# Kernel optimization log

Hardware: AMD Instinct MI355X
Metric: run time of the kernel (lower is better)

Reference implementation:

```python
import jax, jax.numpy as jnp
import numpy as np

B, C, H, W = 4, 128, 64, 64
NUM_HEADS = 4
HEAD_DIM = C // NUM_HEADS


def setup_inputs() -> dict:
    key = jax.random.key(0)
    ks = jax.random.split(key, 9)
    s = 0.02
    return {
        "x": jax.random.normal(ks[0], (B, C, H, W), dtype=jnp.float32),
        "wq": jax.random.normal(ks[1], (C, C), dtype=jnp.float32) * s,
        "bq": jax.random.normal(ks[2], (C,), dtype=jnp.float32) * s,
        "wk": jax.random.normal(ks[3], (C, C), dtype=jnp.float32) * s,
        "bk": jax.random.normal(ks[4], (C,), dtype=jnp.float32) * s,
        "wv": jax.random.normal(ks[5], (C, C), dtype=jnp.float32) * s,
        "bv": jax.random.normal(ks[6], (C,), dtype=jnp.float32) * s,
        "wo": jax.random.normal(ks[7], (C, C), dtype=jnp.float32) * s,
        "bo": jax.random.normal(ks[8], (C,), dtype=jnp.float32) * s,
    }


def _proj(w, b, xf):
    # 1x1 conv == channel-mixing linear: xf is (B, C, N)
    return jnp.einsum("oc,bcn->bon", w, xf) + b[None, :, None]


def reference(x, wq, bq, wk, bk, wv, bv, wo, bo):
    b, c, h, w = x.shape
    n = h * w
    nh, hd = NUM_HEADS, HEAD_DIM
    xf = x.reshape(b, c, n)
    q = _proj(wq, bq, xf).reshape(b, nh, hd, n)
    k = _proj(wk, bk, xf).reshape(b, nh, hd, n)
    v = _proj(wv, bv, xf).reshape(b, nh, hd, n)
    # scores: (b, heads, n, n)
    scores = jnp.einsum("bhdn,bhdm->bhnm", q, k) / jnp.sqrt(jnp.float32(hd)).astype(x.dtype)
    prob = jax.nn.softmax(scores, axis=-1)
    # attn_out: (b, heads, head_dim, n)
    attn = jnp.einsum("bhnm,bhdm->bhdn", prob, v).reshape(b, c, n)
    out = _proj(wo, bo, attn).reshape(b, c, h, w)
    return x + out
```

## Files before the change

### kernel.cpp

```cpp
#include <hip/hip_runtime.h>
#include <hip/hip_bf16.h>

#define BB 4
#define CC 128
#define NN 4096
#define NHEAD 4
#define HDIM 32
#define KSPLIT 2

typedef short bf16x8_t __attribute__((ext_vector_type(8)));
typedef float f32x4_t __attribute__((ext_vector_type(4)));
typedef int i32x4_t __attribute__((ext_vector_type(4)));

#define MFMA16(a, b, c) __builtin_amdgcn_mfma_f32_16x16x32_bf16(a, b, c, 0, 0, 0)
#define EXP2(x) __builtin_amdgcn_exp2f(x)

#define QSCALE (0.17677669529663687f * 1.4426950408889634f)

static __device__ inline unsigned short f2bf(float f) {
  unsigned u = __builtin_bit_cast(unsigned, f);
  u += 0x7fffu + ((u >> 16) & 1u);
  return (unsigned short)(u >> 16);
}
static __device__ inline unsigned pk2(float lo, float hi) {
  return (unsigned)f2bf(lo) | ((unsigned)f2bf(hi) << 16);
}
static __device__ inline unsigned pack_trunc(float lo, float hi) {
  return __builtin_amdgcn_perm(__builtin_bit_cast(unsigned, hi),
                               __builtin_bit_cast(unsigned, lo), 0x07060302u);
}

static __device__ inline void gload_lds16(const unsigned short* gsrc, void* ldst) {
  __builtin_amdgcn_global_load_lds(
      (const __attribute__((address_space(1))) unsigned int*)gsrc,
      (__attribute__((address_space(3))) unsigned int*)ldst, 16, 0, 0);
}

__global__ __launch_bounds__(256) void wconv_kernel(
    const float* __restrict__ wq, const float* __restrict__ wk,
    const float* __restrict__ wv, const float* __restrict__ wo,
    unsigned short* __restrict__ wb) {
  int f = (blockIdx.x * 256 + threadIdx.x) * 8;
  int m = f >> 14, off = f & 16383;
  const float* src = (m == 0) ? wq : (m == 1) ? wk : (m == 2) ? wv : wo;
  float sc = (m == 0) ? QSCALE : 1.0f;
  float4 a = *(const float4*)(src + off);
  float4 b = *(const float4*)(src + off + 4);
  ushort4 u0, u1;
  u0.x = f2bf(a.x * sc); u0.y = f2bf(a.y * sc); u0.z = f2bf(a.z * sc); u0.w = f2bf(a.w * sc);
  u1.x = f2bf(b.x * sc); u1.y = f2bf(b.y * sc); u1.z = f2bf(b.z * sc); u1.w = f2bf(b.w * sc);
  *(ushort4*)(wb + f) = u0;
  *(ushort4*)(wb + f + 4) = u1;
}

__global__ __launch_bounds__(256) void qkv_mfma_kernel(
    const float* __restrict__ x,
    const unsigned short* __restrict__ wqb, const unsigned short* __restrict__ wkb,
    const unsigned short* __restrict__ wvb,
    const float* __restrict__ bq, const float* __restrict__ bk,
    const float* __restrict__ bv,
    unsigned short* __restrict__ qt, unsigned short* __restrict__ kt,
    unsigned short* __restrict__ vg) {
  __shared__ __attribute__((aligned(16))) unsigned short xsb[64][136];
  __shared__ unsigned short vt[128][66];
  const int b = blockIdx.y, nt = blockIdx.x, proj = blockIdx.z;
  const int tid = threadIdx.x;

#pragma unroll
  for (int i = 0; i < 8; i++) {
    int f = tid + 256 * i;
    int c = f >> 4, n4 = (f & 15) * 4;
    float4 v4 = *(const float4*)(x + ((size_t)b * CC + c) * NN + nt * 64 + n4);
    xsb[n4 + 0][c] = f2bf(v4.x);
    xsb[n4 + 1][c] = f2bf(v4.y);
    xsb[n4 + 2][c] = f2bf(v4.z);
    xsb[n4 + 3][c] = f2bf(v4.w);
  }
  __syncthreads();

  const int lane = tid & 63, w = tid >> 6;
  const int l16 = lane & 15, g = lane >> 4;
  const int nl = w * 16;
  const int ngl = nt * 64 + nl;

  bf16x8_t xf[4];
#pragma unroll
  for (int ks = 0; ks < 4; ks++)
    xf[ks] = *(const bf16x8_t*)&xsb[nl + l16][ks * 32 + g * 8];

  const unsigned short* wm = (proj == 0) ? wqb : (proj == 1) ? wkb : wvb;
  const float* bias = (proj == 0) ? bq : (proj == 1) ? bk : bv;
  const float bsc = (proj == 0) ? QSCALE : 1.0f;
  unsigned short* qkdst = proj ? kt : qt;

#pragma unroll
  for (int ot = 0; ot < 8; ot++) {
    f32x4_t acc;
#pragma unroll
    for (int r = 0; r < 4; r++) acc[r] = bias[ot * 16 + g * 4 + r] * bsc;
#pragma unroll
    for (int ks = 0; ks < 4; ks++) {
      bf16x8_t wf = *(const bf16x8_t*)(wm + (size_t)(ot * 16 + l16) * CC + ks * 32 + g * 8);
      acc = MFMA16(wf, xf[ks], acc);
    }
    if (proj < 2) {
      unsigned p0 = pk2(acc[0], acc[1]);
      unsigned p1 = pk2(acc[2], acc[3]);
      unsigned q0 = (unsigned)__shfl_xor((int)p0, 16);
      unsigned q1 = (unsigned)__shfl_xor((int)p1, 16);
      if ((g & 1) == 0) {
        int hh = ot >> 1, dblk = (ot & 1) * 2 + (g >> 1);
        unsigned short* dst =
            qkdst + (((size_t)(b * NHEAD + hh) * 4 + dblk) * NN + ngl + l16) * 8;
        uint4 val = make_uint4(p0, p1, q0, q1);
        *(uint4*)dst = val;
      }
    } else {
#pragma unroll
      for (int r = 0; r < 4; r++) vt[ot * 16 + g * 4 + r][nl + l16] = f2bf(acc[r]);
    }
  }

  if (proj == 2) {
    __syncthreads();
#pragma unroll
    for (int c = 0; c < 4; c++) {
      int cid = c * 256 + tid;
      int hh = cid >> 8, inner = cid & 255;
      int g2 = inner & 3, l16v = (inner >> 2) & 15, fh = inner >> 6;
      int fv = fh >> 1, half = fh & 1;
      int o = hh * 32 + half * 16 + l16v;
      int n0 = fv * 32 + g2 * 4;
      unsigned d0 = *(const unsigned*)&vt[o][n0];
      unsigned d1 = *(const unsigned*)&vt[o][n0 + 2];
      unsigned d2 = *(const unsigned*)&vt[o][n0 + 16];
      unsigned d3 = *(const unsigned*)&vt[o][n0 + 18];
      uint4 val = make_uint4(d0, d1, d2, d3);
      *(uint4*)(vg + (((size_t)(b * NHEAD + hh) * 64 + nt) * 256 + inner) * 8) = val;
    }
  }
}

__global__ __launch_bounds__(256, 4) void attn_mfma5_kernel(
    const unsigned short* __restrict__ qt, const unsigned short* __restrict__ kt,
    const unsigned short* __restrict__ vg,
    float* __restrict__ opart, float* __restrict__ lpart) {
  __shared__ __attribute__((aligned(16))) unsigned short smem[2][4096];

  const int chunk = blockIdx.x & (KSPLIT - 1), nt = blockIdx.x / KSPLIT;
  const int h = blockIdx.y, b = blockIdx.z;
  const int bh = b * NHEAD + h;
  const int tid = threadIdx.x, lane = tid & 63, wid = tid >> 6;
  const int l16 = lane & 15, g = lane >> 4;
  const int nbase = nt * 128 + wid * 32;

  const unsigned short* qb = qt + (size_t)bh * NN * HDIM;
  const unsigned short* kb = kt + (size_t)bh * NN * HDIM;
  const unsigned short* vgb = vg + (size_t)bh * 64 * 2048;

  const bf16x8_t qf0 = *(const bf16x8_t*)(qb + ((size_t)g * NN + nbase + l16) * 8);
  const bf16x8_t qf1 = *(const bf16x8_t*)(qb + ((size_t)g * NN + nbase + 16 + l16) * 8);

  f32x4_t o00 = {0, 0, 0, 0}, o01 = {0, 0, 0, 0};
  f32x4_t o10 = {0, 0, 0, 0}, o11 = {0, 0, 0, 0};
  f32x4_t la = {0, 0, 0, 0}, lb = {0, 0, 0, 0};
  const f32x4_t zf = {0, 0, 0, 0};
  const i32x4_t onesi = {0x3F803F80, 0x3F803F80, 0x3F803F80, 0x3F803F80};
  const bf16x8_t ones = __builtin_bit_cast(bf16x8_t, onesi);

  const int NITER = 64 / KSPLIT;
  const int mt0 = chunk * NITER;

  const unsigned short* ksrc = kb + ((size_t)g * NN + mt0 * 64 + wid * 16 + l16) * 8;
  const unsigned short* vsrc = vgb + (size_t)mt0 * 2048 + (size_t)((wid * 16 + l16) * 4 + g) * 8;

  auto stage = [&](int p, int i) {
    gload_lds16(ksrc + (size_t)i * 512, &smem[p][wid * 512]);
    gload_lds16(vsrc + (size_t)i * 2048, &smem[p][2048 + wid * 512]);
  };

  auto body = [&](int p) {
    const unsigned short* sk = &smem[p][0];
    bf16x8_t k0 = *(const bf16x8_t*)(sk + 0 * 512 + lane * 8);
    bf16x8_t k1 = *(const bf16x8_t*)(sk + 1 * 512 + lane * 8);
    bf16x8_t k2 = *(const bf16x8_t*)(sk + 2 * 512 + lane * 8);
    bf16x8_t k3 = *(const bf16x8_t*)(sk + 3 * 512 + lane * 8);
    bf16x8_t vf0 = *(const bf16x8_t*)(sk + 2048 + 0 * 512 + lane * 8);
    bf16x8_t vf2 = *(const bf16x8_t*)(sk + 2048 + 1 * 512 + lane * 8);
    bf16x8_t vf1 = *(const bf16x8_t*)(sk + 2048 + 2 * 512 + lane * 8);
    bf16x8_t vf3 = *(const bf16x8_t*)(sk + 2048 + 3 * 512 + lane * 8);

    f32x4_t sA0 = MFMA16(k0, qf0, zf), sA1 = MFMA16(k1, qf0, zf);
    f32x4_t sA2 = MFMA16(k2, qf0, zf), sA3 = MFMA16(k3, qf0, zf);
    f32x4_t sB0 = MFMA16(k0, qf1, zf), sB1 = MFMA16(k1, qf1, zf);
    f32x4_t sB2 = MFMA16(k2, qf1, zf), sB3 = MFMA16(k3, qf1, zf);

#pragma unroll
    for (int r = 0; r < 4; r++) {
      sA0[r] = EXP2(sA0[r]); sA1[r] = EXP2(sA1[r]);
      sA2[r] = EXP2(sA2[r]); sA3[r] = EXP2(sA3[r]);
      sB0[r] = EXP2(sB0[r]); sB1[r] = EXP2(sB1[r]);
      sB2[r] = EXP2(sB2[r]); sB3[r] = EXP2(sB3[r]);
    }

    i32x4_t pA0i = {(int)pack_trunc(sA0[0], sA0[1]), (int)pack_trunc(sA0[2], sA0[3]),
                    (int)pack_trunc(sA1[0], sA1[1]), (int)pack_trunc(sA1[2], sA1[3])};
    i32x4_t pA1i = {(int)pack_trunc(sA2[0], sA2[1]), (int)pack_trunc(sA2[2], sA2[3]),
                    (int)pack_trunc(sA3[0], sA3[1]), (int)pack_trunc(sA3[2], sA3[3])};
    i32x4_t pB0i = {(int)pack_trunc(sB0[0], sB0[1]), (int)pack_trunc(sB0[2], sB0[3]),
                    (int)pack_trunc(sB1[0], sB1[1]), (int)pack_trunc(sB1[2], sB1[3])};
    i32x4_t pB1i = {(int)pack_trunc(sB2[0], sB2[1]), (int)pack_trunc(sB2[2], sB2[3]),
                    (int)pack_trunc(sB3[0], sB3[1]), (int)pack_trunc(sB3[2], sB3[3])};
    bf16x8_t pA0 = __builtin_bit_cast(bf16x8_t, pA0i);
    bf16x8_t pA1 = __builtin_bit_cast(bf16x8_t, pA1i);
    bf16x8_t pB0 = __builtin_bit_cast(bf16x8_t, pB0i);
    bf16x8_t pB1 = __builtin_bit_cast(bf16x8_t, pB1i);

    o00 = MFMA16(vf0, pA0, o00); o00 = MFMA16(vf1, pA1, o00);
    o01 = MFMA16(vf2, pA0, o01); o01 = MFMA16(vf3, pA1, o01);
    o10 = MFMA16(vf0, pB0, o10); o10 = MFMA16(vf1, pB1, o10);
    o11 = MFMA16(vf2, pB0, o11); o11 = MFMA16(vf3, pB1, o11);

    la = MFMA16(ones, pA0, la); la = MFMA16(ones, pA1, la);
    lb = MFMA16(ones, pB0, lb); lb = MFMA16(ones, pB1, lb);
  };

  stage(0, 0);
  __syncthreads();
  for (int mi = 0; mi < NITER; mi += 2) {
    stage(1, mi + 1);
    body(0);
    __syncthreads();
    if (mi + 2 < NITER) stage(0, mi + 2);
    body(1);
    __syncthreads();
  }

  float* obase = opart + ((size_t)(chunk * BB * NHEAD + bh)) * HDIM * NN;
#pragma unroll
  for (int r = 0; r < 4; r++) {
    obase[(size_t)(g * 4 + r) * NN + nbase + l16] = o00[r];
    obase[(size_t)(16 + g * 4 + r) * NN + nbase + l16] = o01[r];
    obase[(size_t)(g * 4 + r) * NN + nbase + 16 + l16] = o10[r];
    obase[(size_t)(16 + g * 4 + r) * NN + nbase + 16 + l16] = o11[r];
  }
  if (g == 0) {
    float* lb_ = lpart + (size_t)(chunk * BB * NHEAD + bh) * NN;
    lb_[nbase + l16] = la[0];
    lb_[nbase + 16 + l16] = lb[0];
  }
}

__global__ __launch_bounds__(256) void combine_kernel(
    const float* __restrict__ opart, const float* __restrict__ lpart,
    unsigned short* __restrict__ attnT) {
  const int n = blockIdx.x * 256 + threadIdx.x;
  const int bh = blockIdx.y, dg = blockIdx.z;
  const int b = bh >> 2, h = bh & 3;

  float l = 0.f;
#pragma unroll
  for (int c = 0; c < KSPLIT; c++) l += lpart[(size_t)(c * BB * NHEAD + bh) * NN + n];
  float inv = 1.f / l;

  unsigned dw[4];
#pragma unroll
  for (int p = 0; p < 4; p++) {
    float s0 = 0.f, s1 = 0.f;
#pragma unroll
    for (int c = 0; c < KSPLIT; c++) {
      const float* ob = opart + ((size_t)(c * BB * NHEAD + bh) * HDIM + dg * 8) * NN;
      s0 += ob[(size_t)(2 * p) * NN + n];
      s1 += ob[(size_t)(2 * p + 1) * NN + n];
    }
    dw[p] = (unsigned)f2bf(s0 * inv) | ((unsigned)f2bf(s1 * inv) << 16);
  }
  unsigned short* dst = attnT + ((size_t)b * NN + n) * CC + h * HDIM + dg * 8;
  *(uint4*)dst = *(uint4*)&dw[0];
}

__global__ __launch_bounds__(256) void out_mfma_kernel(
    const unsigned short* __restrict__ attnT, const unsigned short* __restrict__ wob,
    const float* __restrict__ bo, const float* __restrict__ x,
    float* __restrict__ out) {
  const int b = blockIdx.y, nt = blockIdx.x, quarter = blockIdx.z;
  const int tid = threadIdx.x, lane = tid & 63, w = tid >> 6;
  const int l16 = lane & 15, g = lane >> 4;
  const int n0 = nt * 64 + w * 16;

  bf16x8_t bf[4];
#pragma unroll
  for (int ks = 0; ks < 4; ks++)
    bf[ks] = *(const bf16x8_t*)(attnT + ((size_t)b * NN + n0 + l16) * CC + ks * 32 + g * 8);

#pragma unroll
  for (int mi = 0; mi < 2; mi++) {
    int mt = quarter * 2 + mi;
    f32x4_t acc;
#pragma unroll
    for (int r = 0; r < 4; r++) acc[r] = bo[mt * 16 + g * 4 + r];
#pragma unroll
    for (int ks = 0; ks < 4; ks++) {
      bf16x8_t af = *(const bf16x8_t*)(wob + (size_t)(mt * 16 + l16) * CC + ks * 32 + g * 8);
      acc = MFMA16(af, bf[ks], acc);
    }
#pragma unroll
    for (int r = 0; r < 4; r++) {
      int o = mt * 16 + g * 4 + r;
      size_t addr = ((size_t)b * CC + o) * NN + n0 + l16;
      out[addr] = acc[r] + x[addr];
    }
  }
}

extern "C" void kernel_launch(void* const* d_in, const int* in_sizes, int n_in,
                              void* d_out, int out_size, void* d_ws, size_t ws_size,
                              hipStream_t stream) {
  const float* x  = (const float*)d_in[0];
  const float* wq = (const float*)d_in[1];
  const float* bq = (const float*)d_in[2];
  const float* wk = (const float*)d_in[3];
  const float* bk = (const float*)d_in[4];
  const float* wv = (const float*)d_in[5];
  const float* bv = (const float*)d_in[6];
  const float* wo = (const float*)d_in[7];
  const float* bo = (const float*)d_in[8];
  float* out = (float*)d_out;

  char* w = (char*)d_ws;
  const size_t SZ = (size_t)BB * NHEAD * NN * HDIM * 2;
  unsigned short* qt    = (unsigned short*)w;
  unsigned short* kt    = (unsigned short*)(w + SZ);
  unsigned short* vg    = (unsigned short*)(w + 2 * SZ);
  unsigned short* wb    = (unsigned short*)(w + 3 * SZ);
  float* opart = (float*)(w + 3 * SZ + 131072);
  float* lpart = (float*)(w + 3 * SZ + 131072 +
                          (size_t)KSPLIT * BB * NHEAD * HDIM * NN * 4);
  unsigned short* attnT = qt;
  unsigned short* wqb = wb, *wkb = wb + 16384, *wvb = wb + 32768, *wob = wb + 49152;

  wconv_kernel<<<32, 256, 0, stream>>>(wq, wk, wv, wo, wb);
  qkv_mfma_kernel<<<dim3(NN / 64, BB, 3), 256, 0, stream>>>(
      x, wqb, wkb, wvb, bq, bk, bv, qt, kt, vg);
  attn_mfma5_kernel<<<dim3((NN / 128) * KSPLIT, NHEAD, BB), 256, 0, stream>>>(
      qt, kt, vg, opart, lpart);
  combine_kernel<<<dim3(NN / 256, BB * NHEAD, 4), 256, 0, stream>>>(opart, lpart, attnT);
  out_mfma_kernel<<<dim3(NN / 64, BB, 4), 256, 0, stream>>>(attnT, wob, bo, x, out);
}
```

Measured before the change: 148.4 us.

## Raise attention key split, store bf16 partials, sum row-sums on VALU, halve QKV blocks

The attention key dimension is now split four ways instead of two, and occupancy is raised to 8 blocks per CU so more work is in flight. Partial outputs are stored as packed bf16 pairs instead of fp32, which halves partial-buffer traffic at some cost in precision. Softmax row sums are now accumulated with scalar adds and lane shuffles instead of extra MFMAs against a ones vector. The QKV projection grid is doubled, with each block computing half the output channels, and the combine kernel is rewritten to read the packed layout. This adds more split partials to combine and needs tighter register use under the higher occupancy bound.

```diff
diff --git a/kernel.cpp b/kernel.cpp
--- a/kernel.cpp
+++ b/kernel.cpp
@@ -6,7 +6,7 @@
 #define NN 4096
 #define NHEAD 4
 #define HDIM 32
-#define KSPLIT 2
+#define KSPLIT 4
 
 typedef short bf16x8_t __attribute__((ext_vector_type(8)));
 typedef float f32x4_t __attribute__((ext_vector_type(4)));
@@ -28,6 +28,12 @@
 static __device__ inline unsigned pack_trunc(float lo, float hi) {
   return __builtin_amdgcn_perm(__builtin_bit_cast(unsigned, hi),
                                __builtin_bit_cast(unsigned, lo), 0x07060302u);
+}
+static __device__ inline float bfu_lo(unsigned v) {
+  return __builtin_bit_cast(float, v << 16);
+}
+static __device__ inline float bfu_hi(unsigned v) {
+  return __builtin_bit_cast(float, v & 0xFFFF0000u);
 }
 
 static __device__ inline void gload_lds16(const unsigned short* gsrc, void* ldst) {
@@ -62,8 +68,9 @@
     unsigned short* __restrict__ qt, unsigned short* __restrict__ kt,
     unsigned short* __restrict__ vg) {
   __shared__ __attribute__((aligned(16))) unsigned short xsb[64][136];
-  __shared__ unsigned short vt[128][66];
-  const int b = blockIdx.y, nt = blockIdx.x, proj = blockIdx.z;
+  __shared__ unsigned short vt[64][66];
+  const int b = blockIdx.y, nt = blockIdx.x;
+  const int proj = blockIdx.z >> 1, half = blockIdx.z & 1;
   const int tid = threadIdx.x;
 
 #pragma unroll
@@ -94,7 +101,8 @@
   unsigned short* qkdst = proj ? kt : qt;
 
 #pragma unroll
-  for (int ot = 0; ot < 8; ot++) {
+  for (int i = 0; i < 4; i++) {
+    const int ot = half * 4 + i;
     f32x4_t acc;
 #pragma unroll
     for (int r = 0; r < 4; r++) acc[r] = bias[ot * 16 + g * 4 + r] * bsc;
@@ -117,34 +125,35 @@
       }
     } else {
 #pragma unroll
-      for (int r = 0; r < 4; r++) vt[ot * 16 + g * 4 + r][nl + l16] = f2bf(acc[r]);
+      for (int r = 0; r < 4; r++) vt[i * 16 + g * 4 + r][nl + l16] = f2bf(acc[r]);
     }
   }
 
   if (proj == 2) {
     __syncthreads();
 #pragma unroll
-    for (int c = 0; c < 4; c++) {
+    for (int c = 0; c < 2; c++) {
       int cid = c * 256 + tid;
-      int hh = cid >> 8, inner = cid & 255;
+      int hh_l = cid >> 8, inner = cid & 255;
+      int hh = half * 2 + hh_l;
       int g2 = inner & 3, l16v = (inner >> 2) & 15, fh = inner >> 6;
-      int fv = fh >> 1, half = fh & 1;
-      int o = hh * 32 + half * 16 + l16v;
+      int fv = fh >> 1, halfv = fh & 1;
+      int o_l = hh_l * 32 + halfv * 16 + l16v;
       int n0 = fv * 32 + g2 * 4;
-      unsigned d0 = *(const unsigned*)&vt[o][n0];
-      unsigned d1 = *(const unsigned*)&vt[o][n0 + 2];
-      unsigned d2 = *(const unsigned*)&vt[o][n0 + 16];
-      unsigned d3 = *(const unsigned*)&vt[o][n0 + 18];
+      unsigned d0 = *(const unsigned*)&vt[o_l][n0];
+      unsigned d1 = *(const unsigned*)&vt[o_l][n0 + 2];
+      unsigned d2 = *(const unsigned*)&vt[o_l][n0 + 16];
+      unsigned d3 = *(const unsigned*)&vt[o_l][n0 + 18];
       uint4 val = make_uint4(d0, d1, d2, d3);
       *(uint4*)(vg + (((size_t)(b * NHEAD + hh) * 64 + nt) * 256 + inner) * 8) = val;
     }
   }
 }
 
-__global__ __launch_bounds__(256, 4) void attn_mfma5_kernel(
+__global__ __launch_bounds__(256, 8) void attn_mfma6_kernel(
     const unsigned short* __restrict__ qt, const unsigned short* __restrict__ kt,
     const unsigned short* __restrict__ vg,
-    float* __restrict__ opart, float* __restrict__ lpart) {
+    unsigned* __restrict__ obf, float* __restrict__ lpart) {
   __shared__ __attribute__((aligned(16))) unsigned short smem[2][4096];
 
   const int chunk = blockIdx.x & (KSPLIT - 1), nt = blockIdx.x / KSPLIT;
@@ -163,10 +172,8 @@
 
   f32x4_t o00 = {0, 0, 0, 0}, o01 = {0, 0, 0, 0};
   f32x4_t o10 = {0, 0, 0, 0}, o11 = {0, 0, 0, 0};
-  f32x4_t la = {0, 0, 0, 0}, lb = {0, 0, 0, 0};
+  float lA = 0.f, lB = 0.f;
   const f32x4_t zf = {0, 0, 0, 0};
-  const i32x4_t onesi = {0x3F803F80, 0x3F803F80, 0x3F803F80, 0x3F803F80};
-  const bf16x8_t ones = __builtin_bit_cast(bf16x8_t, onesi);
 
   const int NITER = 64 / KSPLIT;
   const int mt0 = chunk * NITER;
@@ -201,6 +208,8 @@
       sA2[r] = EXP2(sA2[r]); sA3[r] = EXP2(sA3[r]);
       sB0[r] = EXP2(sB0[r]); sB1[r] = EXP2(sB1[r]);
       sB2[r] = EXP2(sB2[r]); sB3[r] = EXP2(sB3[r]);
+      lA += (sA0[r] + sA1[r]) + (sA2[r] + sA3[r]);
+      lB += (sB0[r] + sB1[r]) + (sB2[r] + sB3[r]);
     }
 
     i32x4_t pA0i = {(int)pack_trunc(sA0[0], sA0[1]), (int)pack_trunc(sA0[2], sA0[3]),
@@ -220,9 +229,6 @@
     o01 = MFMA16(vf2, pA0, o01); o01 = MFMA16(vf3, pA1, o01);
     o10 = MFMA16(vf0, pB0, o10); o10 = MFMA16(vf1, pB1, o10);
     o11 = MFMA16(vf2, pB0, o11); o11 = MFMA16(vf3, pB1, o11);
-
-    la = MFMA16(ones, pA0, la); la = MFMA16(ones, pA1, la);
-    lb = MFMA16(ones, pB0, lb); lb = MFMA16(ones, pB1, lb);
   };
 
   stage(0, 0);
@@ -236,47 +242,64 @@
     __syncthreads();
   }
 
-  float* obase = opart + ((size_t)(chunk * BB * NHEAD + bh)) * HDIM * NN;
+  lA += __shfl_xor(lA, 16); lA += __shfl_xor(lA, 32);
+  lB += __shfl_xor(lB, 16); lB += __shfl_xor(lB, 32);
+
+  unsigned* ob = obf + (size_t)(chunk * BB * NHEAD + bh) * 32 * 2048;
+  const int dw = (nbase >> 1) + l16;
 #pragma unroll
   for (int r = 0; r < 4; r++) {
-    obase[(size_t)(g * 4 + r) * NN + nbase + l16] = o00[r];
-    obase[(size_t)(16 + g * 4 + r) * NN + nbase + l16] = o01[r];
-    obase[(size_t)(g * 4 + r) * NN + nbase + 16 + l16] = o10[r];
-    obase[(size_t)(16 + g * 4 + r) * NN + nbase + 16 + l16] = o11[r];
+    ob[(size_t)(g * 4 + r) * 2048 + dw] = pk2(o00[r], o10[r]);
+    ob[(size_t)(16 + g * 4 + r) * 2048 + dw] = pk2(o01[r], o11[r]);
   }
   if (g == 0) {
     float* lb_ = lpart + (size_t)(chunk * BB * NHEAD + bh) * NN;
-    lb_[nbase + l16] = la[0];
-    lb_[nbase + 16 + l16] = lb[0];
+    lb_[nbase + l16] = lA;
+    lb_[nbase + 16 + l16] = lB;
   }
 }
 
 __global__ __launch_bounds__(256) void combine_kernel(
-    const float* __restrict__ opart, const float* __restrict__ lpart,
+    const unsigned* __restrict__ obf, const float* __restrict__ lpart,
     unsigned short* __restrict__ attnT) {
-  const int n = blockIdx.x * 256 + threadIdx.x;
+  const int dw = blockIdx.x * 256 + threadIdx.x;
   const int bh = blockIdx.y, dg = blockIdx.z;
   const int b = bh >> 2, h = bh & 3;
-
-  float l = 0.f;
-#pragma unroll
-  for (int c = 0; c < KSPLIT; c++) l += lpart[(size_t)(c * BB * NHEAD + bh) * NN + n];
-  float inv = 1.f / l;
-
-  unsigned dw[4];
+  const int n0 = ((dw >> 4) << 5) + (dw & 15), n1 = n0 + 16;
+
+  float l0 = 0.f, l1 = 0.f;
+#pragma unroll
+  for (int c = 0; c < KSPLIT; c++) {
+    const float* lp = lpart + (size_t)(c * BB * NHEAD + bh) * NN;
+    l0 += lp[n0];
+    l1 += lp[n1];
+  }
+  float inv0 = 1.f / l0, inv1 = 1.f / l1;
+
+  float s0[8], s1[8];
+#pragma unroll
+  for (int j = 0; j < 8; j++) { s0[j] = 0.f; s1[j] = 0.f; }
+#pragma unroll
+  for (int c = 0; c < KSPLIT; c++) {
+    const unsigned* ob =
+        obf + (size_t)(c * BB * NHEAD + bh) * 32 * 2048 + (size_t)dg * 8 * 2048 + dw;
+#pragma unroll
+    for (int j = 0; j < 8; j++) {
+      unsigned v = ob[(size_t)j * 2048];
+      s0[j] += bfu_lo(v);
+      s1[j] += bfu_hi(v);
+    }
+  }
+  unsigned w0[4], w1[4];
 #pragma unroll
   for (int p = 0; p < 4; p++) {
-    float s0 = 0.f, s1 = 0.f;
-#pragma unroll
-    for (int c = 0; c < KSPLIT; c++) {
-      const float* ob = opart + ((size_t)(c * BB * NHEAD + bh) * HDIM + dg * 8) * NN;
-      s0 += ob[(size_t)(2 * p) * NN + n];
-      s1 += ob[(size_t)(2 * p + 1) * NN + n];
-    }
-    dw[p] = (unsigned)f2bf(s0 * inv) | ((unsigned)f2bf(s1 * inv) << 16);
-  }
-  unsigned short* dst = attnT + ((size_t)b * NN + n) * CC + h * HDIM + dg * 8;
-  *(uint4*)dst = *(uint4*)&dw[0];
+    w0[p] = pk2(s0[2 * p] * inv0, s0[2 * p + 1] * inv0);
+    w1[p] = pk2(s1[2 * p] * inv1, s1[2 * p + 1] * inv1);
+  }
+  unsigned short* d0 = attnT + ((size_t)b * NN + n0) * CC + h * HDIM + dg * 8;
+  unsigned short* d1 = attnT + ((size_t)b * NN + n1) * CC + h * HDIM + dg * 8;
+  *(uint4*)d0 = *(uint4*)&w0[0];
+  *(uint4*)d1 = *(uint4*)&w1[0];
 }
 
 __global__ __launch_bounds__(256) void out_mfma_kernel(
@@ -333,17 +356,17 @@
   unsigned short* kt    = (unsigned short*)(w + SZ);
   unsigned short* vg    = (unsigned short*)(w + 2 * SZ);
   unsigned short* wb    = (unsigned short*)(w + 3 * SZ);
-  float* opart = (float*)(w + 3 * SZ + 131072);
+  unsigned* obf = (unsigned*)(w + 3 * SZ + 131072);
   float* lpart = (float*)(w + 3 * SZ + 131072 +
-                          (size_t)KSPLIT * BB * NHEAD * HDIM * NN * 4);
+                          (size_t)KSPLIT * BB * NHEAD * HDIM * NN * 2);
   unsigned short* attnT = qt;
   unsigned short* wqb = wb, *wkb = wb + 16384, *wvb = wb + 32768, *wob = wb + 49152;
 
   wconv_kernel<<<32, 256, 0, stream>>>(wq, wk, wv, wo, wb);
-  qkv_mfma_kernel<<<dim3(NN / 64, BB, 3), 256, 0, stream>>>(
+  qkv_mfma_kernel<<<dim3(NN / 64, BB, 6), 256, 0, stream>>>(
       x, wqb, wkb, wvb, bq, bk, bv, qt, kt, vg);
-  attn_mfma5_kernel<<<dim3((NN / 128) * KSPLIT, NHEAD, BB), 256, 0, stream>>>(
-      qt, kt, vg, opart, lpart);
-  combine_kernel<<<dim3(NN / 256, BB * NHEAD, 4), 256, 0, stream>>>(opart, lpart, attnT);
+  attn_mfma6_kernel<<<dim3((NN / 128) * KSPLIT, NHEAD, BB), 256, 0, stream>>>(
+      qt, kt, vg, obf, lpart);
+  combine_kernel<<<dim3(8, BB * NHEAD, 4), 256, 0, stream>>>(obf, lpart, attnT);
   out_mfma_kernel<<<dim3(NN / 64, BB, 4), 256, 0, stream>>>(attnT, wob, bo, x, out);
 }
```

After: 322.0 us. 2.17x slower.
